# Performance work log

Hardware: AMD Instinct MI355X
Metric: run time of the kernel (lower is better)

## Reference

```python
import math
import jax, jax.numpy as jnp
import numpy as np

DRAGON_ITERATIONS = 12
DRAGON_SMOOTHING = 0.1


def _dragon_patterns(iterations=DRAGON_ITERATIONS, smoothing=DRAGON_SMOOTHING):
    """Deterministic (non-learned) Dragon curve patterns, matching torch impl."""
    patterns = [np.array([0.5], dtype=np.float32)]
    kernel = np.ones(3, dtype=np.float32) / 3.0
    for _ in range(1, iterations):
        prev = patterns[-1]
        n = len(prev)
        newp = np.zeros(2 * n + 1, dtype=np.float32)
        newp[:n] = prev
        newp[n] = 0.5
        newp[n + 1:] = 1.0 - prev[::-1]
        if smoothing > 0:
            # conv1d with kernel_size=3, padding=1 (zero pad) == np.convolve 'same'
            newp = np.convolve(newp, kernel, mode='same').astype(np.float32)
        newp = (newp - newp.min()) / (newp.max() - newp.min() + 1e-8)
        patterns.append(newp.astype(np.float32))
    return patterns

_PATTERNS = _dragon_patterns()


def _interp_pattern(seq_len):
    """Linearly interpolate selected dragon pattern to seq_len (static shapes)."""
    it = min(int(math.log2(seq_len)), DRAGON_ITERATIONS - 1)
    pattern = _PATTERNS[it]
    if len(pattern) == seq_len:
        w = pattern.copy()
    else:
        x_old = np.linspace(0.0, 1.0, len(pattern), dtype=np.float64)
        x_new = np.linspace(0.0, 1.0, seq_len, dtype=np.float64)
        w = np.interp(x_new, x_old, pattern.astype(np.float64)).astype(np.float32)
    return it, jnp.asarray(w)


def setup_inputs() -> dict:
    key = jax.random.key(0)
    ks = jax.random.split(key, 8)
    B, S, D = 8, 2048, 512
    query = jax.random.normal(ks[0], (B, S, D), dtype=jnp.float32)
    k = jax.random.normal(ks[1], (B, S, D), dtype=jnp.float32)
    value = jax.random.normal(ks[2], (B, S, D), dtype=jnp.float32)
    pattern_scale = jnp.ones((DRAGON_ITERATIONS,), dtype=jnp.float32)
    pattern_bias = jnp.zeros((DRAGON_ITERATIONS,), dtype=jnp.float32)
    w1 = jax.random.normal(ks[3], (DRAGON_ITERATIONS, 64), dtype=jnp.float32) * (1.0 / math.sqrt(DRAGON_ITERATIONS))
    b1 = jnp.zeros((64,), dtype=jnp.float32)
    w2 = jax.random.normal(ks[4], (64, 1), dtype=jnp.float32) * (1.0 / 8.0)
    b2 = jnp.zeros((1,), dtype=jnp.float32)
    return {"query": query, "key": k, "value": value,
            "pattern_scale": pattern_scale, "pattern_bias": pattern_bias,
            "w1": w1, "b1": b1, "w2": w2, "b2": b2}


def reference(query, key, value, pattern_scale, pattern_bias, w1, b1, w2, b2):
    B, S, D = key.shape
    it, base_w = _interp_pattern(S)
    # learned affine + softplus on dragon weights
    dragon_w = jax.nn.softplus(base_w * pattern_scale[it] + pattern_bias[it])  # [S]
    weighted_keys = key * dragon_w[None, :, None]                              # [B,S,D]
    scores = jnp.einsum('bqd,bkd->bqk', query, weighted_keys) / math.sqrt(D)   # [B,S,S]
    attn = jax.nn.softmax(scores, axis=-1)
    # blend factor from one-hot iteration features through tiny MLP
    feat = jax.nn.one_hot(it, DRAGON_ITERATIONS, dtype=query.dtype)            # [12]
    h = jax.nn.relu(feat @ w1 + b1)
    blend = jax.nn.sigmoid(h @ w2 + b2)                                        # [1]
    blend = blend[0]
    final_attn = blend * attn + (1.0 - blend) / S                              # uniform blend
    out = jnp.einsum('bqk,bkd->bqd', final_attn, value)                        # [B,S,D]
    # original does output.squeeze(1); S>1 so it's a no-op here
    return out
```

## Files before the change

kernel.cpp:

```cpp
#include <hip/hip_runtime.h>
#include <cstdint>

#define DEV __device__ __forceinline__

typedef float f32x4 __attribute__((ext_vector_type(4)));
typedef short s16x8 __attribute__((ext_vector_type(8)));

DEV unsigned short f2bf(float f){
    unsigned u = __builtin_bit_cast(unsigned, f);
    u = u + 0x7fffu + ((u >> 16) & 1u);
    return (unsigned short)(u >> 16);
}
DEV float bf2f(unsigned short h){
    unsigned u = ((unsigned)h) << 16;
    return __builtin_bit_cast(float, u);
}

typedef const void __attribute__((address_space(1)))* gcp;
typedef void __attribute__((address_space(3)))* lp;
DEV void gload_lds16(const void* g, void* l){
    __builtin_amdgcn_global_load_lds((gcp)g, (lp)l, 16, 0, 0);
}

__global__ __launch_bounds__(256) void k_stage1(
    const float* __restrict__ Q, const float* __restrict__ V,
    const float* __restrict__ scale, const float* __restrict__ bias,
    const float* __restrict__ w1, const float* __restrict__ b1,
    const float* __restrict__ w2, const float* __restrict__ b2,
    float* __restrict__ dragon_w, float* __restrict__ blend_out,
    unsigned short* __restrict__ Qb, unsigned short* __restrict__ Vt,
    float* __restrict__ vmean_part)
{
    __shared__ float sh[8704];
    int tid = threadIdx.x;
    int bx  = blockIdx.x;

    if (bx == 0){
        float* A    = sh;
        float* Bb   = sh + 4096;
        float* sred = sh + 8192;
        if (tid == 0) A[0] = 0.5f;
        __syncthreads();
        int len = 1;
        for (int it = 1; it < 12; ++it){
            int n = len, nl = 2*n + 1;
            for (int i = tid; i < nl; i += 256){
                float v;
                if (i < n)       v = A[i];
                else if (i == n) v = 0.5f;
                else             v = 1.0f - A[2*n - i];
                Bb[i] = v;
            }
            __syncthreads();
            const float third = 1.0f/3.0f;
            for (int i = tid; i < nl; i += 256){
                float s = Bb[i]*third;
                if (i > 0)    s += Bb[i-1]*third;
                if (i < nl-1) s += Bb[i+1]*third;
                A[i] = s;
            }
            __syncthreads();
            float mn = 3.4e38f, mx = -3.4e38f;
            for (int i = tid; i < nl; i += 256){ float v = A[i]; mn = fminf(mn,v); mx = fmaxf(mx,v); }
            sred[tid] = mn; sred[256 + tid] = mx;
            __syncthreads();
            for (int off = 128; off > 0; off >>= 1){
                if (tid < off){
                    sred[tid]       = fminf(sred[tid],       sred[tid+off]);
                    sred[256 + tid] = fmaxf(sred[256 + tid], sred[256 + tid + off]);
                }
                __syncthreads();
            }
            float lo = sred[0], den = sred[256] - lo + 1e-8f;
            for (int i = tid; i < nl; i += 256) A[i] = (A[i] - lo) / den;
            len = nl;
            __syncthreads();
        }
        float sc = scale[11], bi = bias[11];
        for (int i = tid; i < 2048; i += 256){
            float x = A[2*i]*sc + bi;
            dragon_w[i] = fmaxf(x, 0.f) + log1pf(__expf(-fabsf(x)));
        }
        if (tid < 64){
            float h = fmaxf(w1[11*64 + tid] + b1[tid], 0.f);
            float c = h * w2[tid];
            for (int off = 32; off > 0; off >>= 1) c += __shfl_xor(c, off, 64);
            if (tid == 0) blend_out[0] = 1.f/(1.f + __expf(-(c + b2[0])));
        }
        return;
    }

    if (bx <= 2048){
        const long long total4 = (long long)8*2048*512/4;
        long long stride = 2048LL*256;
        for (long long i = (long long)(bx-1)*256 + tid; i < total4; i += stride){
            long long base = i*4;
            const float4 q = *(const float4*)(Q + base);
            ushort4 qo;
            qo.x = f2bf(q.x); qo.y = f2bf(q.y); qo.z = f2bf(q.z); qo.w = f2bf(q.w);
            *(ushort4*)(Qb + base) = qo;
        }
        return;
    }

    int t = bx - 2049;
    int stile = t & 31, dtile = (t >> 5) & 7, b = t >> 8;
    int s0 = stile*64, d0 = dtile*64;
    float (*tile)[67] = (float(*)[67])sh;
    float* red = sh + 4288;
    int c4 = tid & 15, rr = tid >> 4;
    const float* src = V + ((long long)b*2048 + s0)*512 + d0;
    #pragma unroll
    for (int p = 0; p < 4; ++p){
        int row = p*16 + rr;
        const float4 v = *(const float4*)(src + (long long)row*512 + c4*4);
        tile[row][c4*4+0] = v.x; tile[row][c4*4+1] = v.y;
        tile[row][c4*4+2] = v.z; tile[row][c4*4+3] = v.w;
    }
    __syncthreads();
    unsigned short* dst = Vt + ((long long)b*512 + d0)*2048 + s0;
    #pragma unroll
    for (int p = 0; p < 4; ++p){
        int d = p*16 + rr;
        ushort4 o;
        o.x = f2bf(tile[c4*4+0][d]);
        o.y = f2bf(tile[c4*4+1][d]);
        o.z = f2bf(tile[c4*4+2][d]);
        o.w = f2bf(tile[c4*4+3][d]);
        *(ushort4*)(dst + (long long)d*2048 + c4*4) = o;
    }
    int dcol = tid & 63, sp = tid >> 6;
    float s = 0.f;
    #pragma unroll
    for (int ii = 0; ii < 16; ++ii) s += tile[sp*16 + ii][dcol];
    red[sp*64 + dcol] = s;
    __syncthreads();
    if (sp == 0){
        float tot = red[dcol] + red[64+dcol] + red[128+dcol] + red[192+dcol];
        vmean_part[stile*4096 + b*512 + d0 + dcol] = tot * (1.0f/2048.0f);
    }
}

__global__ __launch_bounds__(256) void k_stage2(
    const float* __restrict__ K, const float* __restrict__ dragon_w,
    const float* __restrict__ vmean_part,
    unsigned short* __restrict__ Kb, float* __restrict__ vmean)
{
    int bx = blockIdx.x, tid = threadIdx.x;
    if (bx < 16){
        int idx = bx*256 + tid;
        float s = 0.f;
        #pragma unroll
        for (int st = 0; st < 32; ++st) s += vmean_part[st*4096 + idx];
        vmean[idx] = s;
        return;
    }
    const long long total4 = (long long)8*2048*512/4;
    long long stride = 2048LL*256;
    for (long long i = (long long)(bx-16)*256 + tid; i < total4; i += stride){
        long long base = i*4;
        int s = (int)((base >> 9) & 2047);
        float w = dragon_w[s];
        const float4 k = *(const float4*)(K + base);
        ushort4 ko;
        ko.x = f2bf(k.x*w); ko.y = f2bf(k.y*w); ko.z = f2bf(k.z*w); ko.w = f2bf(k.w*w);
        *(ushort4*)(Kb + base) = ko;
    }
}

#define SCALE_QK 0.04419417382415922f

__global__ __launch_bounds__(256) void k_gemm_qk(
    const unsigned short* __restrict__ Qb, const unsigned short* __restrict__ Kb,
    unsigned short* __restrict__ Sp, float* __restrict__ lpart)
{
    __shared__ unsigned short At[128*64];
    __shared__ unsigned short Bt[128*64];
    int tid = threadIdx.x;
    int lane = tid & 63, wave = tid >> 6;
    int wm = wave >> 1, wn = wave & 1;
    int ln = lane & 15, q4 = lane >> 4;
    int sx = ln & 7;
    int lid = (blockIdx.x & 7)*256 + (blockIdx.x >> 3);
    int kb = lid & 15, qb = (lid >> 4) & 15, b = lid >> 8;
    int q0 = qb*128, k0 = kb*128;
    const unsigned short* Abase = Qb + ((long long)b*2048 + q0)*512;
    const unsigned short* Bbase = Kb + ((long long)b*2048 + k0)*512;

    f32x4 acc[4][4];
    #pragma unroll
    for (int i = 0; i < 4; ++i)
        #pragma unroll
        for (int j = 0; j < 4; ++j) acc[i][j] = (f32x4)0.0f;

    int cc = lane & 7;
    int rg = lane >> 3;
    for (int kt = 0; kt < 8; ++kt){
        #pragma unroll
        for (int c = 0; c < 4; ++c){
            int chunk = wave*4 + c;
            int row = chunk*8 + rg;
            int gc  = cc ^ (row & 7);
            gload_lds16(Abase + (long long)row*512 + kt*64 + gc*8, &At[chunk*512]);
            gload_lds16(Bbase + (long long)row*512 + kt*64 + gc*8, &Bt[chunk*512]);
        }
        __syncthreads();
        #pragma unroll
        for (int ks = 0; ks < 2; ++ks){
            s16x8 af[4], bfr[4];
            int cs = ((ks*4 + q4) ^ sx) * 8;
            #pragma unroll
            for (int i = 0; i < 4; ++i)
                af[i] = *(const s16x8*)&At[(wm*64 + i*16 + ln)*64 + cs];
            #pragma unroll
            for (int j = 0; j < 4; ++j)
                bfr[j] = *(const s16x8*)&Bt[(wn*64 + j*16 + ln)*64 + cs];
            #pragma unroll
            for (int i = 0; i < 4; ++i)
                #pragma unroll
                for (int j = 0; j < 4; ++j)
                    acc[i][j] = __builtin_amdgcn_mfma_f32_16x16x32_bf16(af[i], bfr[j], acc[i][j], 0, 0, 0);
        }
        __syncthreads();
    }
    float* lred = (float*)At;
    unsigned short* outp = Sp + (long long)b*2048*2048;
    #pragma unroll
    for (int i = 0; i < 4; ++i){
        float rs[4] = {0.f, 0.f, 0.f, 0.f};
        #pragma unroll
        for (int j = 0; j < 4; ++j){
            #pragma unroll
            for (int r = 0; r < 4; ++r){
                int q = q0 + wm*64 + i*16 + q4*4 + r;
                int k = k0 + wn*64 + j*16 + ln;
                float v = __expf(acc[i][j][r] * SCALE_QK);
                unsigned short h = f2bf(v);
                outp[(long long)q*2048 + k] = h;
                rs[r] += bf2f(h);
            }
        }
        #pragma unroll
        for (int r = 0; r < 4; ++r){
            float v = rs[r];
            v += __shfl_xor(v, 1, 16);
            v += __shfl_xor(v, 2, 16);
            v += __shfl_xor(v, 4, 16);
            v += __shfl_xor(v, 8, 16);
            if (ln == 0) lred[(wm*64 + i*16 + q4*4 + r)*2 + wn] = v;
        }
    }
    __syncthreads();
    if (tid < 128)
        lpart[((long long)b*16 + kb)*2048 + q0 + tid] = lred[tid*2] + lred[tid*2+1];
}

__global__ __launch_bounds__(256) void k_gemm_pv(
    const unsigned short* __restrict__ Sp, const unsigned short* __restrict__ Vt,
    const float* __restrict__ lpart, const float* __restrict__ vmean,
    const float* __restrict__ blendp, float* __restrict__ out)
{
    __shared__ unsigned short At[128*64];
    __shared__ unsigned short Bt[128*64];
    int tid = threadIdx.x;
    int lane = tid & 63, wave = tid >> 6;
    int wm = wave >> 1, wn = wave & 1;
    int ln = lane & 15, q4 = lane >> 4;
    int sx = ln & 7;
    int lid = (blockIdx.x & 7)*64 + (blockIdx.x >> 3);
    int db = lid & 3, qb = (lid >> 2) & 15, b = lid >> 6;
    int q0 = qb*128, d0 = db*128;
    const unsigned short* Abase = Sp + (long long)b*2048*2048 + (long long)q0*2048;
    const unsigned short* Bbase = Vt + ((long long)b*512 + d0)*2048;

    f32x4 acc[4][4];
    #pragma unroll
    for (int i = 0; i < 4; ++i)
        #pragma unroll
        for (int j = 0; j < 4; ++j) acc[i][j] = (f32x4)0.0f;

    int cc = lane & 7;
    int rg = lane >> 3;
    for (int kt = 0; kt < 32; ++kt){
        #pragma unroll
        for (int c = 0; c < 4; ++c){
            int chunk = wave*4 + c;
            int row = chunk*8 + rg;
            int gc  = cc ^ (row & 7);
            gload_lds16(Abase + (long long)row*2048 + kt*64 + gc*8, &At[chunk*512]);
            gload_lds16(Bbase + (long long)row*2048 + kt*64 + gc*8, &Bt[chunk*512]);
        }
        __syncthreads();
        #pragma unroll
        for (int ks = 0; ks < 2; ++ks){
            s16x8 af[4], bfr[4];
            int cs = ((ks*4 + q4) ^ sx) * 8;
            #pragma unroll
            for (int i = 0; i < 4; ++i)
                af[i] = *(const s16x8*)&At[(wm*64 + i*16 + ln)*64 + cs];
            #pragma unroll
            for (int j = 0; j < 4; ++j)
                bfr[j] = *(const s16x8*)&Bt[(wn*64 + j*16 + ln)*64 + cs];
            #pragma unroll
            for (int i = 0; i < 4; ++i)
                #pragma unroll
                for (int j = 0; j < 4; ++j)
                    acc[i][j] = __builtin_amdgcn_mfma_f32_16x16x32_bf16(af[i], bfr[j], acc[i][j], 0, 0, 0);
        }
        __syncthreads();
    }

    float* l_sh = (float*)Bt;
    if (tid < 128){
        float s = 0.f;
        #pragma unroll
        for (int kb = 0; kb < 16; ++kb)
            s += lpart[((long long)b*16 + kb)*2048 + q0 + tid];
        l_sh[tid] = 1.0f / s;
    }
    __syncthreads();

    float blend = blendp[0];
    float ib = 1.0f - blend;
    float* obase = out + ((long long)b*2048 + q0)*512 + d0;
    float vm[4];
    #pragma unroll
    for (int j = 0; j < 4; ++j) vm[j] = vmean[b*512 + d0 + wn*64 + j*16 + ln];
    #pragma unroll
    for (int i = 0; i < 4; ++i){
        #pragma unroll
        for (int r = 0; r < 4; ++r){
            int ql = wm*64 + i*16 + q4*4 + r;
            float linv = l_sh[ql];
            #pragma unroll
            for (int j = 0; j < 4; ++j){
                int dl = wn*64 + j*16 + ln;
                obase[(long long)ql*512 + dl] = blend*acc[i][j][r]*linv + ib*vm[j];
            }
        }
    }
}

extern "C" void kernel_launch(void* const* d_in, const int* in_sizes, int n_in,
                              void* d_out, int out_size, void* d_ws, size_t ws_size,
                              hipStream_t stream)
{
    (void)in_sizes; (void)n_in; (void)out_size; (void)ws_size;
    const float* Q  = (const float*)d_in[0];
    const float* K  = (const float*)d_in[1];
    const float* V  = (const float*)d_in[2];
    const float* ps = (const float*)d_in[3];
    const float* pb = (const float*)d_in[4];
    const float* w1 = (const float*)d_in[5];
    const float* b1 = (const float*)d_in[6];
    const float* w2 = (const float*)d_in[7];
    const float* b2 = (const float*)d_in[8];
    float* out = (float*)d_out;

    char* ws = (char*)d_ws;
    float* dragon_w        = (float*)(ws);
    float* blend           = (float*)(ws + 8192);
    float* vmean           = (float*)(ws + 16384);
    float* vmean_part      = (float*)(ws + 32768);
    size_t off = 32768 + (size_t)512*1024;
    unsigned short* Qb     = (unsigned short*)(ws + off);
    unsigned short* Kb     = (unsigned short*)(ws + off + (size_t)16*1024*1024);
    unsigned short* Vt     = (unsigned short*)(ws + off + (size_t)32*1024*1024);
    unsigned short* Sp     = (unsigned short*)(ws + off + (size_t)48*1024*1024);
    float* lpart           = (float*)(ws + off + (size_t)112*1024*1024);

    hipLaunchKernelGGL(k_stage1,  dim3(4097), dim3(256), 0, stream,
                       Q, V, ps, pb, w1, b1, w2, b2, dragon_w, blend, Qb, Vt, vmean_part);
    hipLaunchKernelGGL(k_stage2,  dim3(2064), dim3(256), 0, stream,
                       K, dragon_w, vmean_part, Kb, vmean);
    hipLaunchKernelGGL(k_gemm_qk, dim3(2048), dim3(256), 0, stream,
                       Qb, Kb, Sp, lpart);
    hipLaunchKernelGGL(k_gemm_pv, dim3(512),  dim3(256), 0, stream,
                       Sp, Vt, lpart, vmean, blend, out);
}
```

Before: 255.9 us.

## Fold K prep into stage1, apply dragon weights in epilogue, double-buffer GEMMs

The separate k_stage2 launch is removed. K is now converted to bf16 alongside Q in stage1. The per-key dragon weight and the softmax scale are applied to the QK accumulator in the epilogue instead of being multiplied into K beforehand. The vmean reduction moves into the PV kernel's epilogue. Both GEMM kernels now double-buffer their LDS tiles so the next tile's global-to-LDS loads overlap the current tile's MFMAs. This removes one launch and one pass over K, at the cost of doubled LDS per block (which can reduce occupancy) and rounding K to bf16 before scaling instead of after.

Result: faster. 239.2 us (-6.5%).

```diff
diff --git a/kernel.cpp b/kernel.cpp
--- a/kernel.cpp
+++ b/kernel.cpp
@@ -23,13 +23,14 @@
 }
 
 __global__ __launch_bounds__(256) void k_stage1(
-    const float* __restrict__ Q, const float* __restrict__ V,
+    const float* __restrict__ Q, const float* __restrict__ K,
+    const float* __restrict__ V,
     const float* __restrict__ scale, const float* __restrict__ bias,
     const float* __restrict__ w1, const float* __restrict__ b1,
     const float* __restrict__ w2, const float* __restrict__ b2,
     float* __restrict__ dragon_w, float* __restrict__ blend_out,
-    unsigned short* __restrict__ Qb, unsigned short* __restrict__ Vt,
-    float* __restrict__ vmean_part)
+    unsigned short* __restrict__ Qb, unsigned short* __restrict__ Kb,
+    unsigned short* __restrict__ Vt, float* __restrict__ vmean_part)
 {
     __shared__ float sh[8704];
     int tid = threadIdx.x;
@@ -90,20 +91,23 @@
         return;
     }
 
-    if (bx <= 2048){
+    if (bx <= 4096){
+        const float* src = (bx <= 2048) ? Q : K;
+        unsigned short* dst = (bx <= 2048) ? Qb : Kb;
+        int bi = (bx <= 2048) ? (bx-1) : (bx-2049);
         const long long total4 = (long long)8*2048*512/4;
         long long stride = 2048LL*256;
-        for (long long i = (long long)(bx-1)*256 + tid; i < total4; i += stride){
+        for (long long i = (long long)bi*256 + tid; i < total4; i += stride){
             long long base = i*4;
-            const float4 q = *(const float4*)(Q + base);
+            const float4 q = *(const float4*)(src + base);
             ushort4 qo;
             qo.x = f2bf(q.x); qo.y = f2bf(q.y); qo.z = f2bf(q.z); qo.w = f2bf(q.w);
-            *(ushort4*)(Qb + base) = qo;
+            *(ushort4*)(dst + base) = qo;
         }
         return;
     }
 
-    int t = bx - 2049;
+    int t = bx - 4097;
     int stile = t & 31, dtile = (t >> 5) & 7, b = t >> 8;
     int s0 = stile*64, d0 = dtile*64;
     float (*tile)[67] = (float(*)[67])sh;
@@ -141,41 +145,15 @@
     }
 }
 
-__global__ __launch_bounds__(256) void k_stage2(
-    const float* __restrict__ K, const float* __restrict__ dragon_w,
-    const float* __restrict__ vmean_part,
-    unsigned short* __restrict__ Kb, float* __restrict__ vmean)
-{
-    int bx = blockIdx.x, tid = threadIdx.x;
-    if (bx < 16){
-        int idx = bx*256 + tid;
-        float s = 0.f;
-        #pragma unroll
-        for (int st = 0; st < 32; ++st) s += vmean_part[st*4096 + idx];
-        vmean[idx] = s;
-        return;
-    }
-    const long long total4 = (long long)8*2048*512/4;
-    long long stride = 2048LL*256;
-    for (long long i = (long long)(bx-16)*256 + tid; i < total4; i += stride){
-        long long base = i*4;
-        int s = (int)((base >> 9) & 2047);
-        float w = dragon_w[s];
-        const float4 k = *(const float4*)(K + base);
-        ushort4 ko;
-        ko.x = f2bf(k.x*w); ko.y = f2bf(k.y*w); ko.z = f2bf(k.z*w); ko.w = f2bf(k.w*w);
-        *(ushort4*)(Kb + base) = ko;
-    }
-}
-
 #define SCALE_QK 0.04419417382415922f
 
 __global__ __launch_bounds__(256) void k_gemm_qk(
     const unsigned short* __restrict__ Qb, const unsigned short* __restrict__ Kb,
+    const float* __restrict__ dragon_w,
     unsigned short* __restrict__ Sp, float* __restrict__ lpart)
 {
-    __shared__ unsigned short At[128*64];
-    __shared__ unsigned short Bt[128*64];
+    __shared__ unsigned short A0[128*64], B0[128*64];
+    __shared__ unsigned short A1[128*64], B1[128*64];
     int tid = threadIdx.x;
     int lane = tid & 63, wave = tid >> 6;
     int wm = wave >> 1, wn = wave & 1;
@@ -195,16 +173,18 @@
 
     int cc = lane & 7;
     int rg = lane >> 3;
-    for (int kt = 0; kt < 8; ++kt){
+
+    auto STAGE = [&](unsigned short* dA, unsigned short* dB, int kt){
         #pragma unroll
         for (int c = 0; c < 4; ++c){
             int chunk = wave*4 + c;
             int row = chunk*8 + rg;
             int gc  = cc ^ (row & 7);
-            gload_lds16(Abase + (long long)row*512 + kt*64 + gc*8, &At[chunk*512]);
-            gload_lds16(Bbase + (long long)row*512 + kt*64 + gc*8, &Bt[chunk*512]);
-        }
-        __syncthreads();
+            gload_lds16(Abase + (long long)row*512 + kt*64 + gc*8, dA + chunk*512);
+            gload_lds16(Bbase + (long long)row*512 + kt*64 + gc*8, dB + chunk*512);
+        }
+    };
+    auto COMPUTE = [&](const unsigned short* At, const unsigned short* Bt){
         #pragma unroll
         for (int ks = 0; ks < 2; ++ks){
             s16x8 af[4], bfr[4];
@@ -221,9 +201,24 @@
                 for (int j = 0; j < 4; ++j)
                     acc[i][j] = __builtin_amdgcn_mfma_f32_16x16x32_bf16(af[i], bfr[j], acc[i][j], 0, 0, 0);
         }
-        __syncthreads();
-    }
-    float* lred = (float*)At;
+    };
+
+    STAGE(A0, B0, 0); __syncthreads();
+    STAGE(A1, B1, 1); COMPUTE(A0, B0); __syncthreads();
+    STAGE(A0, B0, 2); COMPUTE(A1, B1); __syncthreads();
+    STAGE(A1, B1, 3); COMPUTE(A0, B0); __syncthreads();
+    STAGE(A0, B0, 4); COMPUTE(A1, B1); __syncthreads();
+    STAGE(A1, B1, 5); COMPUTE(A0, B0); __syncthreads();
+    STAGE(A0, B0, 6); COMPUTE(A1, B1); __syncthreads();
+    STAGE(A1, B1, 7); COMPUTE(A0, B0); __syncthreads();
+    COMPUTE(A1, B1); __syncthreads();
+
+    float wj[4];
+    #pragma unroll
+    for (int j = 0; j < 4; ++j)
+        wj[j] = dragon_w[k0 + wn*64 + j*16 + ln] * SCALE_QK;
+
+    float* lred = (float*)A0;
     unsigned short* outp = Sp + (long long)b*2048*2048;
     #pragma unroll
     for (int i = 0; i < 4; ++i){
@@ -234,7 +229,7 @@
             for (int r = 0; r < 4; ++r){
                 int q = q0 + wm*64 + i*16 + q4*4 + r;
                 int k = k0 + wn*64 + j*16 + ln;
-                float v = __expf(acc[i][j][r] * SCALE_QK);
+                float v = __expf(acc[i][j][r] * wj[j]);
                 unsigned short h = f2bf(v);
                 outp[(long long)q*2048 + k] = h;
                 rs[r] += bf2f(h);
@@ -257,11 +252,11 @@
 
 __global__ __launch_bounds__(256) void k_gemm_pv(
     const unsigned short* __restrict__ Sp, const unsigned short* __restrict__ Vt,
-    const float* __restrict__ lpart, const float* __restrict__ vmean,
+    const float* __restrict__ lpart, const float* __restrict__ vmean_part,
     const float* __restrict__ blendp, float* __restrict__ out)
 {
-    __shared__ unsigned short At[128*64];
-    __shared__ unsigned short Bt[128*64];
+    __shared__ unsigned short A0[128*64], B0[128*64];
+    __shared__ unsigned short A1[128*64], B1[128*64];
     int tid = threadIdx.x;
     int lane = tid & 63, wave = tid >> 6;
     int wm = wave >> 1, wn = wave & 1;
@@ -281,16 +276,18 @@
 
     int cc = lane & 7;
     int rg = lane >> 3;
-    for (int kt = 0; kt < 32; ++kt){
+
+    auto STAGE = [&](unsigned short* dA, unsigned short* dB, int kt){
         #pragma unroll
         for (int c = 0; c < 4; ++c){
             int chunk = wave*4 + c;
             int row = chunk*8 + rg;
             int gc  = cc ^ (row & 7);
-            gload_lds16(Abase + (long long)row*2048 + kt*64 + gc*8, &At[chunk*512]);
-            gload_lds16(Bbase + (long long)row*2048 + kt*64 + gc*8, &Bt[chunk*512]);
-        }
-        __syncthreads();
+            gload_lds16(Abase + (long long)row*2048 + kt*64 + gc*8, dA + chunk*512);
+            gload_lds16(Bbase + (long long)row*2048 + kt*64 + gc*8, dB + chunk*512);
+        }
+    };
+    auto COMPUTE = [&](const unsigned short* At, const unsigned short* Bt){
         #pragma unroll
         for (int ks = 0; ks < 2; ++ks){
             s16x8 af[4], bfr[4];
@@ -307,16 +304,31 @@
                 for (int j = 0; j < 4; ++j)
                     acc[i][j] = __builtin_amdgcn_mfma_f32_16x16x32_bf16(af[i], bfr[j], acc[i][j], 0, 0, 0);
         }
-        __syncthreads();
-    }
-
-    float* l_sh = (float*)Bt;
+    };
+
+    STAGE(A0, B0, 0); __syncthreads();
+    for (int kt = 0; kt < 16; ++kt){
+        STAGE(A1, B1, 2*kt + 1);
+        COMPUTE(A0, B0); __syncthreads();
+        if (kt < 15) STAGE(A0, B0, 2*kt + 2);
+        COMPUTE(A1, B1); __syncthreads();
+    }
+
+    float* l_sh  = (float*)A0;
+    float* vm_sh = (float*)B0;
     if (tid < 128){
         float s = 0.f;
         #pragma unroll
         for (int kb = 0; kb < 16; ++kb)
             s += lpart[((long long)b*16 + kb)*2048 + q0 + tid];
         l_sh[tid] = 1.0f / s;
+    } else {
+        int d = tid - 128;
+        float s = 0.f;
+        #pragma unroll
+        for (int st = 0; st < 32; ++st)
+            s += vmean_part[st*4096 + b*512 + d0 + d];
+        vm_sh[d] = s;
     }
     __syncthreads();
 
@@ -325,7 +337,7 @@
     float* obase = out + ((long long)b*2048 + q0)*512 + d0;
     float vm[4];
     #pragma unroll
-    for (int j = 0; j < 4; ++j) vm[j] = vmean[b*512 + d0 + wn*64 + j*16 + ln];
+    for (int j = 0; j < 4; ++j) vm[j] = vm_sh[wn*64 + j*16 + ln];
     #pragma unroll
     for (int i = 0; i < 4; ++i){
         #pragma unroll
@@ -360,7 +372,6 @@
     char* ws = (char*)d_ws;
     float* dragon_w        = (float*)(ws);
     float* blend           = (float*)(ws + 8192);
-    float* vmean           = (float*)(ws + 16384);
     float* vmean_part      = (float*)(ws + 32768);
     size_t off = 32768 + (size_t)512*1024;
     unsigned short* Qb     = (unsigned short*)(ws + off);
@@ -369,12 +380,11 @@
     unsigned short* Sp     = (unsigned short*)(ws + off + (size_t)48*1024*1024);
     float* lpart           = (float*)(ws + off + (size_t)112*1024*1024);
 
-    hipLaunchKernelGGL(k_stage1,  dim3(4097), dim3(256), 0, stream,
-                       Q, V, ps, pb, w1, b1, w2, b2, dragon_w, blend, Qb, Vt, vmean_part);
-    hipLaunchKernelGGL(k_stage2,  dim3(2064), dim3(256), 0, stream,
-                       K, dragon_w, vmean_part, Kb, vmean);
+    hipLaunchKernelGGL(k_stage1,  dim3(6145), dim3(256), 0, stream,
+                       Q, K, V, ps, pb, w1, b1, w2, b2, dragon_w, blend,
+                       Qb, Kb, Vt, vmean_part);
     hipLaunchKernelGGL(k_gemm_qk, dim3(2048), dim3(256), 0, stream,
-                       Qb, Kb, Sp, lpart);
+                       Qb, Kb, dragon_w, Sp, lpart);
     hipLaunchKernelGGL(k_gemm_pv, dim3(512),  dim3(256), 0, stream,
-                       Sp, Vt, lpart, vmean, blend, out);
-}
+                       Sp, Vt, lpart, vmean_part, blend, out);
+}
```
